# Kernel tuning notes

Measured on AMD Instinct MI355X. Metric: run time of the kernel, lower is better.

The kernel has to match this reference:

```python
import jax, jax.numpy as jnp
import numpy as np

N, K, C = 100000, 32, 128  # n_nodes, max_degree, channels


def setup_inputs() -> dict:
    key = jax.random.key(0)
    k1, k2, k3, k4 = jax.random.split(key, 4)
    x = jax.random.normal(k1, (N, C), dtype=jnp.float32)
    edge_index = jax.random.randint(k2, (N, K), 0, N, dtype=jnp.int64)
    # GCNConv uses nn.Linear(in, out, bias=False): weight shape [out, in]
    W1 = jax.random.normal(k3, (C, C), dtype=jnp.float32) / np.sqrt(C)
    W2 = jax.random.normal(k4, (C, C), dtype=jnp.float32) / np.sqrt(C)
    return {"x": x, "edge_index": edge_index, "W1": W1, "W2": W2}


def _gcn_layer(x, edge_index, W):
    # node degree counts valid (>=0) neighbors plus self
    deg = jnp.sum(edge_index >= 0, axis=-1, keepdims=True).astype(x.dtype) + 1.0
    sqrt_deg = jnp.sqrt(deg)
    h = (x @ W.T) / sqrt_deg  # [N, C]
    # pad with a zero row so index -1 (padding) gathers zeros
    padded = jnp.concatenate([h, jnp.zeros((1, h.shape[-1]), h.dtype)], axis=0)
    neigh_sum = padded[edge_index].sum(axis=1)  # [N, K, C] -> [N, C]
    return (neigh_sum + h) / sqrt_deg


def reference(x, edge_index, W1, W2):
    h = jax.nn.elu(_gcn_layer(x, edge_index, W1))
    h = jax.nn.elu(_gcn_layer(h, edge_index, W2))
    return h
```

## Files before the change

### kernel.cpp

```cpp
#include <hip/hip_runtime.h>
#include <hip/hip_bf16.h>
#include <math.h>

namespace {

constexpr int C = 128;
constexpr int K = 32;

typedef float float4v __attribute__((ext_vector_type(4)));
typedef short short8v __attribute__((ext_vector_type(8)));

__device__ __forceinline__ float bf2f(unsigned short u) {
    return __uint_as_float(((unsigned int)u) << 16);
}
__device__ __forceinline__ unsigned short f2bf(float x) {
    __hip_bfloat16 h = __float2bfloat16(x);
    return *(unsigned short*)&h;
}

__global__ __launch_bounds__(256) void deg_kernel(const int* __restrict__ edge,
                                                  float* __restrict__ invs,
                                                  unsigned int* __restrict__ hzero,
                                                  int N) {
    if (blockIdx.x == 0 && threadIdx.x < 64) {
        hzero[(size_t)N * (C / 2) + threadIdx.x] = 0u;
    }
    int t = threadIdx.x;
    int node = blockIdx.x * 8 + (t >> 5);
    int k = t & 31;
    int e = (node < N) ? edge[(size_t)node * K + k] : -1;
    unsigned long long m = __ballot(e >= 0);
    int lane = t & 63;
    unsigned int half = (lane < 32) ? (unsigned int)(m & 0xffffffffULL)
                                    : (unsigned int)(m >> 32);
    int c = __popc(half);
    if (k == 0 && node < N) invs[node] = 1.0f / sqrtf((float)(c + 1));
}

__global__ __launch_bounds__(256, 2) void gemm_mfma_kernel(
    const float* __restrict__ X, const float* __restrict__ W,
    const float* __restrict__ invs, unsigned short* __restrict__ H, int N) {
    __shared__ unsigned short Whl[2][C][136];

    const int t = threadIdx.x;
    const int n0 = blockIdx.x * 128;

    for (int p = t; p < C * C / 4; p += 256) {
        int row = p >> 5;
        int c4 = (p & 31) * 4;
        float4 w = ((const float4*)W)[p];
        float wv[4] = {w.x, w.y, w.z, w.w};
#pragma unroll
        for (int j = 0; j < 4; ++j) {
            unsigned short hb = f2bf(wv[j]);
            Whl[0][row][c4 + j] = hb;
            Whl[1][row][c4 + j] = f2bf(wv[j] - bf2f(hb));
        }
    }
    __syncthreads();

    const int wv = t >> 6;
    const int l = t & 63;
    const int lm = l & 15;
    const int lk = l >> 4;
    const int rbase = n0 + wv * 32;

    int rowA0 = rbase + lm;
    int rowA1 = rbase + 16 + lm;
    rowA0 = rowA0 < N ? rowA0 : N - 1;
    rowA1 = rowA1 < N ? rowA1 : N - 1;
    const float* xp0 = X + (size_t)rowA0 * C;
    const float* xp1 = X + (size_t)rowA1 * C;

    float4v acc[2][8];
#pragma unroll
    for (int rt = 0; rt < 2; ++rt)
#pragma unroll
        for (int ct = 0; ct < 8; ++ct) acc[rt][ct] = {0.f, 0.f, 0.f, 0.f};

#pragma unroll
    for (int ks = 0; ks < 4; ++ks) {
        const int kb = ks * 32 + lk * 8;
        float xr0[8], xr1[8];
        *(float4v*)&xr0[0] = *(const float4v*)(xp0 + kb);
        *(float4v*)&xr0[4] = *(const float4v*)(xp0 + kb + 4);
        *(float4v*)&xr1[0] = *(const float4v*)(xp1 + kb);
        *(float4v*)&xr1[4] = *(const float4v*)(xp1 + kb + 4);
        short8v ah0, al0, ah1, al1;
#pragma unroll
        for (int j = 0; j < 8; ++j) {
            unsigned short h0 = f2bf(xr0[j]);
            unsigned short h1 = f2bf(xr1[j]);
            ah0[j] = (short)h0;
            ah1[j] = (short)h1;
            al0[j] = (short)f2bf(xr0[j] - bf2f(h0));
            al1[j] = (short)f2bf(xr1[j] - bf2f(h1));
        }
#pragma unroll
        for (int ct = 0; ct < 8; ++ct) {
            short8v bh = *(const short8v*)&Whl[0][ct * 16 + lm][kb];
            short8v bl = *(const short8v*)&Whl[1][ct * 16 + lm][kb];
            acc[0][ct] = __builtin_amdgcn_mfma_f32_16x16x32_bf16(ah0, bh,
                                                                 acc[0][ct], 0, 0, 0);
            acc[0][ct] = __builtin_amdgcn_mfma_f32_16x16x32_bf16(al0, bh,
                                                                 acc[0][ct], 0, 0, 0);
            acc[0][ct] = __builtin_amdgcn_mfma_f32_16x16x32_bf16(ah0, bl,
                                                                 acc[0][ct], 0, 0, 0);
            acc[1][ct] = __builtin_amdgcn_mfma_f32_16x16x32_bf16(ah1, bh,
                                                                 acc[1][ct], 0, 0, 0);
            acc[1][ct] = __builtin_amdgcn_mfma_f32_16x16x32_bf16(al1, bh,
                                                                 acc[1][ct], 0, 0, 0);
            acc[1][ct] = __builtin_amdgcn_mfma_f32_16x16x32_bf16(ah1, bl,
                                                                 acc[1][ct], 0, 0, 0);
        }
    }

    float sc[2][4];
#pragma unroll
    for (int rt = 0; rt < 2; ++rt)
#pragma unroll
        for (int q = 0; q < 4; ++q) {
            int r = rbase + rt * 16 + lk * 4 + q;
            sc[rt][q] = invs[r < N ? r : N - 1];
        }
#pragma unroll
    for (int rt = 0; rt < 2; ++rt)
#pragma unroll
        for (int ct = 0; ct < 8; ++ct)
#pragma unroll
            for (int q = 0; q < 4; ++q) {
                int r = rbase + rt * 16 + lk * 4 + q;
                if (r < N)
                    H[(size_t)r * C + ct * 16 + lm] =
                        f2bf(acc[rt][ct][q] * sc[rt][q]);
            }
}

__global__ __launch_bounds__(256) void gather_elu_kernel(
    const unsigned short* __restrict__ H, const int* __restrict__ edge,
    const float* __restrict__ invs, float* __restrict__ out, int N) {
    __shared__ int idx_s[8][K];

    const int t = threadIdx.x;
    const int g = t >> 5;
    const int lane32 = t & 31;
    const int node = blockIdx.x * 8 + g;

    idx_s[g][lane32] = (node < N) ? edge[(size_t)node * K + lane32] : -1;
    __syncthreads();
    if (node >= N) return;

    const unsigned short* hp = H + lane32 * 4;
    float a0 = 0.f, a1 = 0.f, a2 = 0.f, a3 = 0.f;

#pragma unroll
    for (int k0 = 0; k0 < K; k0 += 16) {
        ushort4 v[16];
#pragma unroll
        for (int u = 0; u < 16; ++u) {
            int j = idx_s[g][k0 + u];
            j = (j < 0) ? N : j;
            v[u] = *(const ushort4*)(hp + (size_t)j * C);
        }
#pragma unroll
        for (int u = 0; u < 16; ++u) {
            a0 += bf2f(v[u].x);
            a1 += bf2f(v[u].y);
            a2 += bf2f(v[u].z);
            a3 += bf2f(v[u].w);
        }
    }

    ushort4 sv = *(const ushort4*)(hp + (size_t)node * C);
    float s = invs[node];
    float r0 = (a0 + bf2f(sv.x)) * s;
    float r1 = (a1 + bf2f(sv.y)) * s;
    float r2 = (a2 + bf2f(sv.z)) * s;
    float r3 = (a3 + bf2f(sv.w)) * s;
    r0 = r0 > 0.f ? r0 : expm1f(r0);
    r1 = r1 > 0.f ? r1 : expm1f(r1);
    r2 = r2 > 0.f ? r2 : expm1f(r2);
    r3 = r3 > 0.f ? r3 : expm1f(r3);
    float4v rv = {r0, r1, r2, r3};
    *(float4v*)(out + (size_t)node * C + lane32 * 4) = rv;
}

}

extern "C" void kernel_launch(void* const* d_in, const int* in_sizes, int n_in,
                              void* d_out, int out_size, void* d_ws, size_t ws_size,
                              hipStream_t stream) {
    const float* x = (const float*)d_in[0];
    const int* edge = (const int*)d_in[1];
    const float* W1 = (const float*)d_in[2];
    const float* W2 = (const float*)d_in[3];
    float* out = (float*)d_out;
    const int N = in_sizes[0] / C;

    char* ws = (char*)d_ws;
    float* invs = (float*)ws;
    size_t invs_bytes = ((size_t)N * sizeof(float) + 255) & ~(size_t)255;
    unsigned short* h = (unsigned short*)(ws + invs_bytes);

    const int nodeBlocks = (N + 7) / 8;
    const int gemmBlocks = (N + 127) / 128;

    deg_kernel<<<nodeBlocks, 256, 0, stream>>>(edge, invs, (unsigned int*)h, N);
    gemm_mfma_kernel<<<gemmBlocks, 256, 0, stream>>>(x, W1, invs, h, N);
    gather_elu_kernel<<<nodeBlocks, 256, 0, stream>>>(h, edge, invs, out, N);
    gemm_mfma_kernel<<<gemmBlocks, 256, 0, stream>>>(out, W2, invs, h, N);
    gather_elu_kernel<<<nodeBlocks, 256, 0, stream>>>(h, edge, invs, out, N);
}
```

Before: 279.3 us.

## Precompute split-bf16 weights once, widen gather loads to 16B, vectorize degree count

The degree kernel now also converts both weight matrices into hi/lo bf16 halves in workspace, so each GEMM block copies pre-split weights into LDS instead of converting 16K floats per block. The gather kernel uses 16 lanes per node with 8-element (16-byte) bf16 loads per neighbor row, halving the number of load instructions. Degree counting reads int4 edges and reduces with shuffles. Wider gathers raise per-thread register use and may lower occupancy for the latency-bound gather.

```diff
diff --git a/kernel.cpp b/kernel.cpp
--- a/kernel.cpp
+++ b/kernel.cpp
@@ -9,6 +9,8 @@
 
 typedef float float4v __attribute__((ext_vector_type(4)));
 typedef short short8v __attribute__((ext_vector_type(8)));
+typedef unsigned short ushort8v __attribute__((ext_vector_type(8)));
+typedef int int2v __attribute__((ext_vector_type(2)));
 
 __device__ __forceinline__ float bf2f(unsigned short u) {
     return __uint_as_float(((unsigned int)u) << 16);
@@ -18,44 +20,54 @@
     return *(unsigned short*)&h;
 }
 
-__global__ __launch_bounds__(256) void deg_kernel(const int* __restrict__ edge,
-                                                  float* __restrict__ invs,
-                                                  unsigned int* __restrict__ hzero,
-                                                  int N) {
-    if (blockIdx.x == 0 && threadIdx.x < 64) {
-        hzero[(size_t)N * (C / 2) + threadIdx.x] = 0u;
-    }
-    int t = threadIdx.x;
-    int node = blockIdx.x * 8 + (t >> 5);
-    int k = t & 31;
-    int e = (node < N) ? edge[(size_t)node * K + k] : -1;
-    unsigned long long m = __ballot(e >= 0);
-    int lane = t & 63;
-    unsigned int half = (lane < 32) ? (unsigned int)(m & 0xffffffffULL)
-                                    : (unsigned int)(m >> 32);
-    int c = __popc(half);
-    if (k == 0 && node < N) invs[node] = 1.0f / sqrtf((float)(c + 1));
+__global__ __launch_bounds__(256) void deg_kernel(
+    const int* __restrict__ edge, float* __restrict__ invs,
+    unsigned int* __restrict__ hzero, const float* __restrict__ W1,
+    const float* __restrict__ W2, unsigned short* __restrict__ whl, int N) {
+    const int bid = blockIdx.x;
+    const int t = threadIdx.x;
+
+    if (bid == 0 && t < 64) {
+        hzero[(size_t)N * (C / 2) + t] = 0u;
+    }
+    if (bid >= 1 && bid <= 128) {
+        int which = (bid - 1) >> 6;
+        int p = ((bid - 1) & 63) * 256 + t;
+        float w = (which ? W2 : W1)[p];
+        unsigned short hb = f2bf(w);
+        unsigned short lb = f2bf(w - bf2f(hb));
+        unsigned short* dst = whl + (size_t)which * 32768;
+        dst[p] = hb;
+        dst[16384 + p] = lb;
+    }
+
+    int node = bid * 32 + (t >> 3);
+    int k4 = (t & 7) * 4;
+    int4 e = make_int4(-1, -1, -1, -1);
+    if (node < N) e = *(const int4*)(edge + (size_t)node * K + k4);
+    int cnt = (e.x >= 0) + (e.y >= 0) + (e.z >= 0) + (e.w >= 0);
+    cnt += __shfl_xor(cnt, 1);
+    cnt += __shfl_xor(cnt, 2);
+    cnt += __shfl_xor(cnt, 4);
+    if ((t & 7) == 0 && node < N)
+        invs[node] = 1.0f / sqrtf((float)(cnt + 1));
 }
 
 __global__ __launch_bounds__(256, 2) void gemm_mfma_kernel(
-    const float* __restrict__ X, const float* __restrict__ W,
+    const float* __restrict__ X, const unsigned short* __restrict__ Wp,
     const float* __restrict__ invs, unsigned short* __restrict__ H, int N) {
     __shared__ unsigned short Whl[2][C][136];
 
     const int t = threadIdx.x;
     const int n0 = blockIdx.x * 128;
 
-    for (int p = t; p < C * C / 4; p += 256) {
-        int row = p >> 5;
-        int c4 = (p & 31) * 4;
-        float4 w = ((const float4*)W)[p];
-        float wv[4] = {w.x, w.y, w.z, w.w};
-#pragma unroll
-        for (int j = 0; j < 4; ++j) {
-            unsigned short hb = f2bf(wv[j]);
-            Whl[0][row][c4 + j] = hb;
-            Whl[1][row][c4 + j] = f2bf(wv[j] - bf2f(hb));
-        }
+    for (int p = t; p < 2 * C * 16; p += 256) {
+        int seg = p >> 11;
+        int rem = p & 2047;
+        int row = rem >> 4;
+        int v8 = (rem & 15) * 8;
+        *(ushort8v*)&Whl[seg][row][v8] =
+            *(const ushort8v*)(Wp + (size_t)seg * 16384 + row * 128 + v8);
     }
     __syncthreads();
 
@@ -139,50 +151,59 @@
 __global__ __launch_bounds__(256) void gather_elu_kernel(
     const unsigned short* __restrict__ H, const int* __restrict__ edge,
     const float* __restrict__ invs, float* __restrict__ out, int N) {
-    __shared__ int idx_s[8][K];
+    __shared__ int idx_s[16][K];
 
     const int t = threadIdx.x;
-    const int g = t >> 5;
-    const int lane32 = t & 31;
-    const int node = blockIdx.x * 8 + g;
-
-    idx_s[g][lane32] = (node < N) ? edge[(size_t)node * K + lane32] : -1;
+    const int g = t >> 4;
+    const int l16 = t & 15;
+    const int node = blockIdx.x * 16 + g;
+
+    {
+        int p = t * 2;
+        int r = p >> 5;
+        int c0 = p & 31;
+        int nn = blockIdx.x * 16 + r;
+        int2v e = {-1, -1};
+        if (nn < N) e = *(const int2v*)(edge + (size_t)nn * K + c0);
+        idx_s[r][c0] = e.x;
+        idx_s[r][c0 + 1] = e.y;
+    }
     __syncthreads();
     if (node >= N) return;
 
-    const unsigned short* hp = H + lane32 * 4;
-    float a0 = 0.f, a1 = 0.f, a2 = 0.f, a3 = 0.f;
+    const unsigned short* hp = H + l16 * 8;
+    float acc[8];
+#pragma unroll
+    for (int i = 0; i < 8; ++i) acc[i] = 0.f;
 
 #pragma unroll
     for (int k0 = 0; k0 < K; k0 += 16) {
-        ushort4 v[16];
+        ushort8v v[16];
 #pragma unroll
         for (int u = 0; u < 16; ++u) {
             int j = idx_s[g][k0 + u];
             j = (j < 0) ? N : j;
-            v[u] = *(const ushort4*)(hp + (size_t)j * C);
-        }
-#pragma unroll
-        for (int u = 0; u < 16; ++u) {
-            a0 += bf2f(v[u].x);
-            a1 += bf2f(v[u].y);
-            a2 += bf2f(v[u].z);
-            a3 += bf2f(v[u].w);
-        }
-    }
-
-    ushort4 sv = *(const ushort4*)(hp + (size_t)node * C);
+            v[u] = *(const ushort8v*)(hp + (size_t)j * C);
+        }
+#pragma unroll
+        for (int u = 0; u < 16; ++u)
+#pragma unroll
+            for (int i = 0; i < 8; ++i) acc[i] += bf2f(v[u][i]);
+    }
+
+    ushort8v sv = *(const ushort8v*)(hp + (size_t)node * C);
     float s = invs[node];
-    float r0 = (a0 + bf2f(sv.x)) * s;
-    float r1 = (a1 + bf2f(sv.y)) * s;
-    float r2 = (a2 + bf2f(sv.z)) * s;
-    float r3 = (a3 + bf2f(sv.w)) * s;
-    r0 = r0 > 0.f ? r0 : expm1f(r0);
-    r1 = r1 > 0.f ? r1 : expm1f(r1);
-    r2 = r2 > 0.f ? r2 : expm1f(r2);
-    r3 = r3 > 0.f ? r3 : expm1f(r3);
-    float4v rv = {r0, r1, r2, r3};
-    *(float4v*)(out + (size_t)node * C + lane32 * 4) = rv;
+    float r[8];
+#pragma unroll
+    for (int i = 0; i < 8; ++i) {
+        float x = (acc[i] + bf2f(sv[i])) * s;
+        r[i] = x > 0.f ? x : expm1f(x);
+    }
+    float* dst = out + (size_t)node * C + l16 * 8;
+    float4v lo = {r[0], r[1], r[2], r[3]};
+    float4v hi = {r[4], r[5], r[6], r[7]};
+    *(float4v*)dst = lo;
+    *(float4v*)(dst + 4) = hi;
 }
 
 }
@@ -201,13 +222,17 @@
     float* invs = (float*)ws;
     size_t invs_bytes = ((size_t)N * sizeof(float) + 255) & ~(size_t)255;
     unsigned short* h = (unsigned short*)(ws + invs_bytes);
-
-    const int nodeBlocks = (N + 7) / 8;
+    size_t h_bytes = (((size_t)(N + 1) * C * 2) + 255) & ~(size_t)255;
+    unsigned short* whl = (unsigned short*)(ws + invs_bytes + h_bytes);
+
+    const int degBlocks = (N + 31) / 32;
     const int gemmBlocks = (N + 127) / 128;
-
-    deg_kernel<<<nodeBlocks, 256, 0, stream>>>(edge, invs, (unsigned int*)h, N);
-    gemm_mfma_kernel<<<gemmBlocks, 256, 0, stream>>>(x, W1, invs, h, N);
-    gather_elu_kernel<<<nodeBlocks, 256, 0, stream>>>(h, edge, invs, out, N);
-    gemm_mfma_kernel<<<gemmBlocks, 256, 0, stream>>>(out, W2, invs, h, N);
-    gather_elu_kernel<<<nodeBlocks, 256, 0, stream>>>(h, edge, invs, out, N);
-}
+    const int gatherBlocks = (N + 15) / 16;
+
+    deg_kernel<<<degBlocks, 256, 0, stream>>>(edge, invs, (unsigned int*)h, W1,
+                                              W2, whl, N);
+    gemm_mfma_kernel<<<gemmBlocks, 256, 0, stream>>>(x, whl, invs, h, N);
+    gather_elu_kernel<<<gatherBlocks, 256, 0, stream>>>(h, edge, invs, out, N);
+    gemm_mfma_kernel<<<gemmBlocks, 256, 0, stream>>>(out, whl + 32768, invs, h, N);
+    gather_elu_kernel<<<gatherBlocks, 256, 0, stream>>>(h, edge, invs, out, N);
+}
```

Result: no change. 283.4 us (+1.5%).

## Bucket neighbor indices by node range and stagger gather order per XCD

Applied to the files above, without the earlier changes.

A new prep kernel computes degree scaling, pre-splits both weight matrices into bf16 hi/lo parts once, and counting-sorts each node's neighbor list into 8 buckets by index range. The gather kernel then walks the buckets starting from a block-dependent offset, so concurrent blocks on different XCDs touch different slices of H at the same time. The aim is better L2/MALL locality for the random gathers. It costs an extra sorted-edge buffer, data-dependent loops with less memory-level parallelism than the old 16-wide unrolled loads, and a fallback path when the workspace is too small.

```diff
diff --git a/kernel.cpp b/kernel.cpp
--- a/kernel.cpp
+++ b/kernel.cpp
@@ -6,9 +6,11 @@
 
 constexpr int C = 128;
 constexpr int K = 32;
+constexpr int NB = 8;
 
 typedef float float4v __attribute__((ext_vector_type(4)));
 typedef short short8v __attribute__((ext_vector_type(8)));
+typedef unsigned short ushort8v __attribute__((ext_vector_type(8)));
 
 __device__ __forceinline__ float bf2f(unsigned short u) {
     return __uint_as_float(((unsigned int)u) << 16);
@@ -18,44 +20,85 @@
     return *(unsigned short*)&h;
 }
 
-__global__ __launch_bounds__(256) void deg_kernel(const int* __restrict__ edge,
-                                                  float* __restrict__ invs,
-                                                  unsigned int* __restrict__ hzero,
-                                                  int N) {
-    if (blockIdx.x == 0 && threadIdx.x < 64) {
-        hzero[(size_t)N * (C / 2) + threadIdx.x] = 0u;
-    }
-    int t = threadIdx.x;
-    int node = blockIdx.x * 8 + (t >> 5);
-    int k = t & 31;
-    int e = (node < N) ? edge[(size_t)node * K + k] : -1;
-    unsigned long long m = __ballot(e >= 0);
-    int lane = t & 63;
-    unsigned int half = (lane < 32) ? (unsigned int)(m & 0xffffffffULL)
-                                    : (unsigned int)(m >> 32);
-    int c = __popc(half);
-    if (k == 0 && node < N) invs[node] = 1.0f / sqrtf((float)(c + 1));
+__global__ __launch_bounds__(256) void prep_kernel(
+    const int* __restrict__ edge, int* __restrict__ sedge,
+    unsigned long long* __restrict__ offs, float* __restrict__ invs,
+    unsigned int* __restrict__ hz1, const float* __restrict__ W1,
+    const float* __restrict__ W2, unsigned short* __restrict__ whl, int N,
+    int do_sort) {
+    const int bid = blockIdx.x;
+    const int t = threadIdx.x;
+
+    if (bid == 0 && t < 64) hz1[(size_t)N * (C / 2) + t] = 0u;
+    if (bid >= 1 && bid <= 128) {
+        int which = (bid - 1) >> 6;
+        int p = ((bid - 1) & 63) * 256 + t;
+        float w = (which ? W2 : W1)[p];
+        unsigned short hb = f2bf(w);
+        unsigned short lb = f2bf(w - bf2f(hb));
+        unsigned short* dst = whl + (size_t)which * 32768;
+        dst[p] = hb;
+        dst[16384 + p] = lb;
+    }
+
+    const int node = bid * 256 + t;
+    if (node >= N) return;
+
+    int j[32];
+    const int4* ep = (const int4*)(edge + (size_t)node * K);
+#pragma unroll
+    for (int q = 0; q < 8; ++q) {
+        int4 e = ep[q];
+        j[q * 4 + 0] = e.x;
+        j[q * 4 + 1] = e.y;
+        j[q * 4 + 2] = e.z;
+        j[q * 4 + 3] = e.w;
+    }
+    int valid = 0;
+#pragma unroll
+    for (int k = 0; k < K; ++k) valid += (j[k] >= 0) ? 1 : 0;
+    invs[node] = 1.0f / sqrtf((float)(valid + 1));
+
+    if (!do_sort) return;
+
+    const float binv = 8.0f / (float)(N + 1);
+    int b[32];
+    unsigned long long cnts = 0;
+#pragma unroll
+    for (int k = 0; k < K; ++k) {
+        int jj = j[k] < 0 ? N : j[k];
+        j[k] = jj;
+        int bb = (int)((float)jj * binv);
+        bb = bb > 7 ? 7 : bb;
+        b[k] = bb;
+        cnts += 1ull << (8 * bb);
+    }
+    offs[node] = cnts;
+
+    int* dst = sedge + (size_t)node * K;
+    int pos = 0;
+#pragma unroll
+    for (int bb = 0; bb < NB; ++bb)
+#pragma unroll
+        for (int k = 0; k < K; ++k)
+            if (b[k] == bb) dst[pos++] = j[k];
 }
 
 __global__ __launch_bounds__(256, 2) void gemm_mfma_kernel(
-    const float* __restrict__ X, const float* __restrict__ W,
+    const float* __restrict__ X, const unsigned short* __restrict__ Wp,
     const float* __restrict__ invs, unsigned short* __restrict__ H, int N) {
     __shared__ unsigned short Whl[2][C][136];
 
     const int t = threadIdx.x;
     const int n0 = blockIdx.x * 128;
 
-    for (int p = t; p < C * C / 4; p += 256) {
-        int row = p >> 5;
-        int c4 = (p & 31) * 4;
-        float4 w = ((const float4*)W)[p];
-        float wv[4] = {w.x, w.y, w.z, w.w};
-#pragma unroll
-        for (int j = 0; j < 4; ++j) {
-            unsigned short hb = f2bf(wv[j]);
-            Whl[0][row][c4 + j] = hb;
-            Whl[1][row][c4 + j] = f2bf(wv[j] - bf2f(hb));
-        }
+    for (int p = t; p < 2 * C * 16; p += 256) {
+        int seg = p >> 11;
+        int rem = p & 2047;
+        int row = rem >> 4;
+        int v8 = (rem & 15) * 8;
+        *(ushort8v*)&Whl[seg][row][v8] =
+            *(const ushort8v*)(Wp + (size_t)seg * 16384 + row * 128 + v8);
     }
     __syncthreads();
 
@@ -136,38 +179,62 @@
             }
 }
 
-__global__ __launch_bounds__(256) void gather_elu_kernel(
-    const unsigned short* __restrict__ H, const int* __restrict__ edge,
-    const float* __restrict__ invs, float* __restrict__ out, int N) {
+__global__ __launch_bounds__(256) void gather_elu_b_kernel(
+    const unsigned short* __restrict__ H, const int* __restrict__ sedge,
+    const unsigned long long* __restrict__ offs, const float* __restrict__ invs,
+    float* __restrict__ out, int N) {
     __shared__ int idx_s[8][K];
+    __shared__ int start_s[8][NB + 1];
 
     const int t = threadIdx.x;
     const int g = t >> 5;
     const int lane32 = t & 31;
     const int node = blockIdx.x * 8 + g;
 
-    idx_s[g][lane32] = (node < N) ? edge[(size_t)node * K + lane32] : -1;
+    idx_s[g][lane32] = (node < N) ? sedge[(size_t)node * K + lane32] : N;
+    if (lane32 == 0) {
+        unsigned long long cc = (node < N) ? offs[node] : 0ull;
+        int a = 0;
+#pragma unroll
+        for (int bb = 0; bb < NB; ++bb) {
+            start_s[g][bb] = a;
+            a += (int)((cc >> (8 * bb)) & 255ull);
+        }
+        start_s[g][NB] = a;
+    }
     __syncthreads();
     if (node >= N) return;
 
     const unsigned short* hp = H + lane32 * 4;
     float a0 = 0.f, a1 = 0.f, a2 = 0.f, a3 = 0.f;
-
-#pragma unroll
-    for (int k0 = 0; k0 < K; k0 += 16) {
-        ushort4 v[16];
-#pragma unroll
-        for (int u = 0; u < 16; ++u) {
-            int j = idx_s[g][k0 + u];
-            j = (j < 0) ? N : j;
-            v[u] = *(const ushort4*)(hp + (size_t)j * C);
-        }
-#pragma unroll
-        for (int u = 0; u < 16; ++u) {
-            a0 += bf2f(v[u].x);
-            a1 += bf2f(v[u].y);
-            a2 += bf2f(v[u].z);
-            a3 += bf2f(v[u].w);
+    const int xcd = blockIdx.x & (NB - 1);
+
+#pragma unroll
+    for (int pp = 0; pp < NB; ++pp) {
+        const int p = (xcd + pp) & (NB - 1);
+        int k = start_s[g][p];
+        const int k1 = start_s[g][p + 1];
+        for (; k + 2 <= k1; k += 2) {
+            int j0 = idx_s[g][k];
+            int j1 = idx_s[g][k + 1];
+            ushort4 v0 = *(const ushort4*)(hp + (size_t)j0 * C);
+            ushort4 v1 = *(const ushort4*)(hp + (size_t)j1 * C);
+            a0 += bf2f(v0.x);
+            a1 += bf2f(v0.y);
+            a2 += bf2f(v0.z);
+            a3 += bf2f(v0.w);
+            a0 += bf2f(v1.x);
+            a1 += bf2f(v1.y);
+            a2 += bf2f(v1.z);
+            a3 += bf2f(v1.w);
+        }
+        if (k < k1) {
+            int j0 = idx_s[g][k];
+            ushort4 v0 = *(const ushort4*)(hp + (size_t)j0 * C);
+            a0 += bf2f(v0.x);
+            a1 += bf2f(v0.y);
+            a2 += bf2f(v0.z);
+            a3 += bf2f(v0.w);
         }
     }
 
@@ -185,6 +252,53 @@
     *(float4v*)(out + (size_t)node * C + lane32 * 4) = rv;
 }
 
+__global__ __launch_bounds__(256) void gather_elu_kernel(
+    const unsigned short* __restrict__ H, const int* __restrict__ edge,
+    const float* __restrict__ invs, float* __restrict__ out, int N) {
+    __shared__ int idx_s[8][K];
+
+    const int t = threadIdx.x;
+    const int g = t >> 5;
+    const int lane32 = t & 31;
+    const int node = blockIdx.x * 8 + g;
+
+    idx_s[g][lane32] = (node < N) ? edge[(size_t)node * K + lane32] : -1;
+    __syncthreads();
+    if (node >= N) return;
+
+    const unsigned short* hp = H + lane32 * 4;
+    float a0 = 0.f, a1 = 0.f, a2 = 0.f, a3 = 0.f;
+#pragma unroll
+    for (int k0 = 0; k0 < K; k0 += 16) {
+        ushort4 v[16];
+#pragma unroll
+        for (int u = 0; u < 16; ++u) {
+            int j = idx_s[g][k0 + u];
+            j = (j < 0) ? N : j;
+            v[u] = *(const ushort4*)(hp + (size_t)j * C);
+        }
+#pragma unroll
+        for (int u = 0; u < 16; ++u) {
+            a0 += bf2f(v[u].x);
+            a1 += bf2f(v[u].y);
+            a2 += bf2f(v[u].z);
+            a3 += bf2f(v[u].w);
+        }
+    }
+    ushort4 sv = *(const ushort4*)(hp + (size_t)node * C);
+    float s = invs[node];
+    float r0 = (a0 + bf2f(sv.x)) * s;
+    float r1 = (a1 + bf2f(sv.y)) * s;
+    float r2 = (a2 + bf2f(sv.z)) * s;
+    float r3 = (a3 + bf2f(sv.w)) * s;
+    r0 = r0 > 0.f ? r0 : expm1f(r0);
+    r1 = r1 > 0.f ? r1 : expm1f(r1);
+    r2 = r2 > 0.f ? r2 : expm1f(r2);
+    r3 = r3 > 0.f ? r3 : expm1f(r3);
+    float4v rv = {r0, r1, r2, r3};
+    *(float4v*)(out + (size_t)node * C + lane32 * 4) = rv;
+}
+
 }
 
 extern "C" void kernel_launch(void* const* d_in, const int* in_sizes, int n_in,
@@ -198,16 +312,45 @@
     const int N = in_sizes[0] / C;
 
     char* ws = (char*)d_ws;
+    const size_t invs_bytes = ((size_t)N * sizeof(float) + 255) & ~(size_t)255;
+    const size_t h_bytes = (((size_t)(N + 1) * C * 2) + 255) & ~(size_t)255;
+    const size_t whl_bytes = 2 * 2 * 16384 * sizeof(unsigned short);
+    const size_t sedge_bytes = (((size_t)N * K * 4) + 255) & ~(size_t)255;
+    const size_t offs_bytes = (size_t)N * 8;
+
     float* invs = (float*)ws;
-    size_t invs_bytes = ((size_t)N * sizeof(float) + 255) & ~(size_t)255;
-    unsigned short* h = (unsigned short*)(ws + invs_bytes);
-
-    const int nodeBlocks = (N + 7) / 8;
+    unsigned short* h1 = (unsigned short*)(ws + invs_bytes);
+    unsigned short* whl = (unsigned short*)(ws + invs_bytes + h_bytes);
+
+    const int prepBlocks = (N + 255) / 256;
     const int gemmBlocks = (N + 127) / 128;
-
-    deg_kernel<<<nodeBlocks, 256, 0, stream>>>(edge, invs, (unsigned int*)h, N);
-    gemm_mfma_kernel<<<gemmBlocks, 256, 0, stream>>>(x, W1, invs, h, N);
-    gather_elu_kernel<<<nodeBlocks, 256, 0, stream>>>(h, edge, invs, out, N);
-    gemm_mfma_kernel<<<gemmBlocks, 256, 0, stream>>>(out, W2, invs, h, N);
-    gather_elu_kernel<<<nodeBlocks, 256, 0, stream>>>(h, edge, invs, out, N);
-}
+    const int gatherBlocks = (N + 7) / 8;
+
+    const bool bucketed =
+        ws_size >= invs_bytes + h_bytes + whl_bytes + sedge_bytes + offs_bytes;
+
+    if (bucketed) {
+        int* sedge = (int*)(ws + invs_bytes + h_bytes + whl_bytes);
+        unsigned long long* offs =
+            (unsigned long long*)(ws + invs_bytes + h_bytes + whl_bytes +
+                                  sedge_bytes);
+
+        prep_kernel<<<prepBlocks, 256, 0, stream>>>(
+            edge, sedge, offs, invs, (unsigned int*)h1, W1, W2, whl, N, 1);
+        gemm_mfma_kernel<<<gemmBlocks, 256, 0, stream>>>(x, whl, invs, h1, N);
+        gather_elu_b_kernel<<<gatherBlocks, 256, 0, stream>>>(h1, sedge, offs,
+                                                              invs, out, N);
+        gemm_mfma_kernel<<<gemmBlocks, 256, 0, stream>>>(out, whl + 32768, invs,
+                                                         h1, N);
+        gather_elu_b_kernel<<<gatherBlocks, 256, 0, stream>>>(h1, sedge, offs,
+                                                              invs, out, N);
+    } else {
+        prep_kernel<<<prepBlocks, 256, 0, stream>>>(
+            edge, nullptr, nullptr, invs, (unsigned int*)h1, W1, W2, whl, N, 0);
+        gemm_mfma_kernel<<<gemmBlocks, 256, 0, stream>>>(x, whl, invs, h1, N);
+        gather_elu_kernel<<<gatherBlocks, 256, 0, stream>>>(h1, edge, invs, out, N);
+        gemm_mfma_kernel<<<gemmBlocks, 256, 0, stream>>>(out, whl + 32768, invs,
+                                                         h1, N);
+        gather_elu_kernel<<<gatherBlocks, 256, 0, stream>>>(h1, edge, invs, out, N);
+    }
+}
```

Result: slower. 301.8 us (+8.0%).
